# Optimization experiments

Hardware: AMD Instinct MI355X
Metric: run time of the kernel (lower is better)

Reference implementation:

```python
import jax, jax.numpy as jnp
import numpy as np

HEADS = 4
DIM_HEAD = 32


def setup_inputs() -> dict:
    key = jax.random.key(0)
    k1, k2, k3, k4 = jax.random.split(key, 4)
    dim = 128
    hidden = HEADS * DIM_HEAD  # 128
    x = jax.random.normal(k1, (32, dim, 64, 64), dtype=jnp.float32)
    w_qkv = jax.random.normal(k2, (3 * hidden, dim), dtype=jnp.float32) * (1.0 / np.sqrt(dim))
    w_out = jax.random.normal(k3, (dim, hidden), dtype=jnp.float32) * (1.0 / np.sqrt(hidden))
    b_out = jax.random.normal(k4, (dim,), dtype=jnp.float32) * 0.01
    return {"x": x, "w_qkv": w_qkv, "w_out": w_out, "b_out": b_out}


def reference(x, w_qkv, w_out, b_out):
    b, c, h, w = x.shape
    n = h * w
    # 1x1 conv (no bias) == channel matmul
    qkv = jnp.einsum('oc,bchw->bohw', w_qkv, x)  # [b, 3*heads*dh, h, w]
    qkv = qkv.reshape(b, 3, HEADS, DIM_HEAD, n)
    q, k, v = qkv[:, 0], qkv[:, 1], qkv[:, 2]  # each [b, heads, dh, n]
    k = jax.nn.softmax(k, axis=-1)  # softmax over spatial positions
    context = jnp.einsum('bhdn,bhen->bhde', k, v)  # [b, heads, dh, dh]
    out = jnp.einsum('bhde,bhdn->bhen', context, q)  # [b, heads, dh, n]
    out = out.reshape(b, HEADS * DIM_HEAD, h, w)
    # 1x1 conv with bias
    return jnp.einsum('oc,bchw->bohw', w_out, out) + b_out[None, :, None, None]
```

## Files before the change

kernel.cpp:

```cpp
#include <hip/hip_runtime.h>
#include <hip/hip_bf16.h>
#include <math.h>

#define BATCH 32
#define CDIM  128
#define NTOT  4096
#define NCH   32
#define CHN   128
#define TN    64
#define NCH3  16

typedef __attribute__((ext_vector_type(4))) float f32x4;
typedef __attribute__((ext_vector_type(8))) short s16x8;

#define PC_OFF  0
#define PC_SIZE (BATCH * 4 * NCH * 32 * 32)
#define PS_OFF  (PC_OFF + PC_SIZE)
#define PS_SIZE (BATCH * 4 * NCH * 32)
#define MBF_OFF (PS_OFF + PS_SIZE)
#define MBF_SIZE (BATCH * CDIM * CDIM / 2)
#define CTX_OFF (MBF_OFF + MBF_SIZE)
#define CTX_SIZE (BATCH * 4 * 1024)
#define XBT_OFF (CTX_OFF + CTX_SIZE)
#define XBT_SIZE (BATCH * CDIM * NTOT / 2)
#define NEED_BYTES ((size_t)(XBT_OFF + XBT_SIZE) * 4)

static __device__ __forceinline__ unsigned short f2bf(float f) {
    return __builtin_bit_cast(unsigned short, __float2bfloat16(f));
}
static __device__ __forceinline__ unsigned int pack2(float a, float b) {
    return (unsigned int)f2bf(a) | ((unsigned int)f2bf(b) << 16);
}
static __device__ __forceinline__ s16x8 ld_frag_lds(const unsigned int* p, int d0) {
    int4 t;
    t.x = (int)p[d0]; t.y = (int)p[d0 + 1];
    t.z = (int)p[d0 + 2]; t.w = (int)p[d0 + 3];
    return __builtin_bit_cast(s16x8, t);
}

static __device__ __forceinline__ void stage_xT(const float* __restrict__ xc,
                                                unsigned int* __restrict__ xsd,
                                                int tid) {
    const int m  = tid & 15;
    const int cg = tid >> 4;
#pragma unroll
    for (int p = 0; p < 4; ++p) {
        const int c = 2 * cg + 32 * p;
        const f32x4 a0 = *reinterpret_cast<const f32x4*>(xc + (size_t)c * NTOT + 4 * m);
        const f32x4 a1 = *reinterpret_cast<const f32x4*>(xc + (size_t)(c + 1) * NTOT + 4 * m);
#pragma unroll
        for (int jj = 0; jj < 4; ++jj)
            xsd[(4 * m + jj) * 65 + (c >> 1)] = pack2(a0[jj], a1[jj]);
    }
}

template <bool XBT>
__global__ __launch_bounds__(256, 2)
void k1_ctx(const float* __restrict__ x, const float* __restrict__ wqkv,
            float* __restrict__ ws) {
    __shared__ __attribute__((aligned(16))) unsigned short xsT[64 * 130];
    __shared__ __attribute__((aligned(16))) unsigned short ekv[8][32][72];

    const int j = blockIdx.x, b = blockIdx.y;
    const int tid = threadIdx.x;
    const int l = tid & 63;
    const int w = tid >> 6;
    const int m = l & 15, hq = l >> 4;

    s16x8 afr[4][4];
#pragma unroll
    for (int tm = 0; tm < 4; ++tm)
#pragma unroll
        for (int kt = 0; kt < 4; ++kt) {
            const float* wr = wqkv +
                (size_t)(CDIM + 64 * w + 16 * tm + m) * CDIM + 32 * kt + 8 * hq;
            const f32x4 u0 = *reinterpret_cast<const f32x4*>(wr);
            const f32x4 u1 = *reinterpret_cast<const f32x4*>(wr + 4);
            int4 t4;
            t4.x = (int)pack2(u0[0], u0[1]); t4.y = (int)pack2(u0[2], u0[3]);
            t4.z = (int)pack2(u1[0], u1[1]); t4.w = (int)pack2(u1[2], u1[3]);
            afr[tm][kt] = __builtin_bit_cast(s16x8, t4);
        }

    f32x4 cacc[2][2] = {};
    float sacc[4][4] = {};
    const float* xc = x + (size_t)b * CDIM * NTOT + j * CHN;
    unsigned int* xsd = (unsigned int*)xsT;

    for (int it = 0; it < CHN / TN; ++it) {
        stage_xT(xc + it * TN, xsd, tid);
        __syncthreads();

        f32x4 acc[4][4] = {};
#pragma unroll
        for (int kt = 0; kt < 4; ++kt) {
#pragma unroll
            for (int tn = 0; tn < 4; ++tn) {
                const s16x8 bfr = ld_frag_lds(xsd, (16 * tn + m) * 65 + 16 * kt + 4 * hq);
#pragma unroll
                for (int tm = 0; tm < 4; ++tm)
                    acc[tm][tn] = __builtin_amdgcn_mfma_f32_16x16x32_bf16(
                        afr[tm][kt], bfr, acc[tm][tn], 0, 0, 0);
            }
        }

        if constexpr (XBT) {
            unsigned int* tb = (unsigned int*)(ws + XBT_OFF) +
                               ((size_t)b * 64 + j * 2 + it) * 4096;
            const int n = tid >> 2, qt = tid & 3;
#pragma unroll
            for (int p = 0; p < 4; ++p) {
                const int cdl = 16 * p + 4 * qt;
                const int src = n * 65 + (cdl ^ ((n & 7) << 2));
                uint4 v;
                v.x = xsd[src]; v.y = xsd[src + 1];
                v.z = xsd[src + 2]; v.w = xsd[src + 3];
                *reinterpret_cast<uint4*>(tb + (size_t)n * 64 + cdl) = v;
            }
        }

        if (w < 2) {
#pragma unroll
            for (int tm = 0; tm < 4; ++tm)
#pragma unroll
                for (int tn = 0; tn < 4; ++tn)
#pragma unroll
                    for (int r = 0; r < 4; ++r) {
                        const int dg = 64 * w + 16 * tm + 4 * hq + r;
                        const float e = __expf(acc[tm][tn][r]);
                        sacc[tm][r] += e;
                        ekv[dg >> 5][dg & 31][16 * tn + m] = f2bf(e);
                    }
        } else {
#pragma unroll
            for (int tm = 0; tm < 4; ++tm)
#pragma unroll
                for (int tn = 0; tn < 4; ++tn)
#pragma unroll
                    for (int r = 0; r < 4; ++r) {
                        const int eg = 64 * (w - 2) + 16 * tm + 4 * hq + r;
                        ekv[4 + (eg >> 5)][eg & 31][16 * tn + m] = f2bf(acc[tm][tn][r]);
                    }
        }
        __syncthreads();

#pragma unroll
        for (int kt = 0; kt < 2; ++kt) {
            s16x8 va[2], eb[2];
#pragma unroll
            for (int t = 0; t < 2; ++t) {
                va[t] = *reinterpret_cast<const s16x8*>(
                    &ekv[4 + w][16 * t + m][32 * kt + 8 * hq]);
                eb[t] = *reinterpret_cast<const s16x8*>(
                    &ekv[w][16 * t + m][32 * kt + 8 * hq]);
            }
#pragma unroll
            for (int tm = 0; tm < 2; ++tm)
#pragma unroll
                for (int tn = 0; tn < 2; ++tn)
                    cacc[tm][tn] = __builtin_amdgcn_mfma_f32_16x16x32_bf16(
                        va[tm], eb[tn], cacc[tm][tn], 0, 0, 0);
        }
        __syncthreads();
    }

    float* pc = ws + PC_OFF + (size_t)((b * 4 + w) * NCH + j) * 1024;
#pragma unroll
    for (int tm = 0; tm < 2; ++tm)
#pragma unroll
        for (int tn = 0; tn < 2; ++tn)
#pragma unroll
            for (int r = 0; r < 4; ++r)
                pc[(16 * tm + 4 * hq + r) * 32 + 16 * tn + m] = cacc[tm][tn][r];

    if (w < 2) {
#pragma unroll
        for (int tm = 0; tm < 4; ++tm)
#pragma unroll
            for (int r = 0; r < 4; ++r) {
                float s = sacc[tm][r];
                s += __shfl_xor(s, 1);
                s += __shfl_xor(s, 2);
                s += __shfl_xor(s, 4);
                s += __shfl_xor(s, 8);
                if (m == 0) {
                    const int dg = 64 * w + 16 * tm + 4 * hq + r;
                    ws[PS_OFF + (size_t)((b * 4 + (dg >> 5)) * NCH + j) * 32 + (dg & 31)] = s;
                }
            }
    }
}

__global__ __launch_bounds__(256)
void k2a_ctx(float* __restrict__ ws) {
    const int bh = blockIdx.x;
    const int tid = threadIdx.x;
    __shared__ float stotS[32];
    if (tid < 32) {
        float s = 0.f;
#pragma unroll 8
        for (int jj = 0; jj < NCH; ++jj)
            s += ws[PS_OFF + (size_t)(bh * NCH + jj) * 32 + tid];
        stotS[tid] = s;
    }
    __syncthreads();
#pragma unroll
    for (int k = 0; k < 4; ++k) {
        const int idx = tid + 256 * k;
        float c = 0.f;
#pragma unroll 8
        for (int jj = 0; jj < NCH; ++jj)
            c += ws[PC_OFF + (size_t)(bh * NCH + jj) * 1024 + idx];
        ws[CTX_OFF + (size_t)bh * 1024 + idx] = c / stotS[idx & 31];
    }
}

__global__ __launch_bounds__(256)
void k2b_buildM(const float* __restrict__ wqkv, const float* __restrict__ wout,
                float* __restrict__ ws) {
    const int oq = blockIdx.x;
    const int b  = blockIdx.y;
    const int tid = threadIdx.x;

    __shared__ __attribute__((aligned(16))) float smA[8704];
    __shared__ float G[32][133];
    float* ctxs  = smA;
    float* wouts = smA + 4224;
    unsigned int* wqs = (unsigned int*)smA;

#pragma unroll
    for (int k = 0; k < 16; ++k) {
        const int fid = tid + 256 * k;
        const int h = fid >> 10, rem = fid & 1023;
        const int e = rem >> 5, d = rem & 31;
        ctxs[(h * 32 + d) * 33 + e] = ws[CTX_OFF + (size_t)b * 4096 + fid];
    }
#pragma unroll
    for (int k = 0; k < 16; ++k) {
        const int fid = tid + 256 * k;
        const int o = fid >> 7, c = fid & 127;
        wouts[o * 133 + c] = wout[(size_t)(oq * 32 + o) * CDIM + c];
    }
    __syncthreads();

    {
        const int o2 = tid & 31;
        const int g8 = tid >> 5;
#pragma unroll
        for (int i = 0; i < 16; ++i) {
            const int hd = g8 * 16 + i;
            const int h = hd >> 5;
            float acc = 0.f;
#pragma unroll
            for (int e = 0; e < 32; ++e)
                acc = fmaf(wouts[o2 * 133 + h * 32 + e], ctxs[hd * 33 + e], acc);
            G[o2][hd] = acc;
        }
    }
    __syncthreads();

    {
#pragma unroll
        for (int k = 0; k < 32; ++k) {
            const int fid = tid + 256 * k;
            const int hd = fid >> 6, cd = fid & 63;
            const float2 wv =
                *reinterpret_cast<const float2*>(wqkv + (size_t)hd * CDIM + 2 * cd);
            wqs[hd * 68 + cd] = pack2(wv.x, wv.y);
        }
    }
    __syncthreads();

    {
        const int o3 = tid >> 3;
        const int c0 = tid & 7;
        float Macc[16];
#pragma unroll
        for (int i = 0; i < 16; ++i) Macc[i] = 0.f;
        for (int hd = 0; hd < 128; ++hd) {
            const float gv = G[o3][hd];
            const uint4 w0 = *reinterpret_cast<const uint4*>(&wqs[hd * 68 + c0 * 8]);
            const uint4 w1 = *reinterpret_cast<const uint4*>(&wqs[hd * 68 + c0 * 8 + 4]);
            const unsigned int dw[8] = {w0.x, w0.y, w0.z, w0.w, w1.x, w1.y, w1.z, w1.w};
#pragma unroll
            for (int q = 0; q < 8; ++q) {
                const float lo = __builtin_bit_cast(float, dw[q] << 16);
                const float hi = __builtin_bit_cast(float, dw[q] & 0xffff0000u);
                Macc[2 * q]     = fmaf(gv, lo, Macc[2 * q]);
                Macc[2 * q + 1] = fmaf(gv, hi, Macc[2 * q + 1]);
            }
        }
        unsigned int* mpd = (unsigned int*)((unsigned short*)(ws + MBF_OFF) +
                                            (size_t)b * CDIM * CDIM) +
                            (oq * 32 + o3) * 64 + c0 * 8;
        uint4 s0, s1;
        s0.x = pack2(Macc[0], Macc[1]);   s0.y = pack2(Macc[2], Macc[3]);
        s0.z = pack2(Macc[4], Macc[5]);   s0.w = pack2(Macc[6], Macc[7]);
        s1.x = pack2(Macc[8], Macc[9]);   s1.y = pack2(Macc[10], Macc[11]);
        s1.z = pack2(Macc[12], Macc[13]); s1.w = pack2(Macc[14], Macc[15]);
        *reinterpret_cast<uint4*>(mpd) = s0;
        *reinterpret_cast<uint4*>(mpd + 4) = s1;
    }
}

template <bool XBT>
__global__ __launch_bounds__(256)
void k3_final(const float* __restrict__ x, const float* __restrict__ bout,
              const float* __restrict__ ws, float* __restrict__ out) {
    __shared__ __attribute__((aligned(16))) unsigned int xsd[4160];

    const int j = blockIdx.x, b = blockIdx.y;
    const int tid = threadIdx.x, l = tid & 63, w = tid >> 6;
    const int m = l & 15, hq = l >> 4;

    const unsigned short* mbf =
        (const unsigned short*)(ws + MBF_OFF) + (size_t)b * CDIM * CDIM;
    s16x8 afr[2][4];
#pragma unroll
    for (int tm = 0; tm < 2; ++tm)
#pragma unroll
        for (int kt = 0; kt < 4; ++kt)
            afr[tm][kt] = *reinterpret_cast<const s16x8*>(
                mbf + (size_t)(32 * w + 16 * tm + m) * CDIM + 32 * kt + 8 * hq);
    float bias[2][4];
#pragma unroll
    for (int tm = 0; tm < 2; ++tm)
#pragma unroll
        for (int r = 0; r < 4; ++r)
            bias[tm][r] = bout[32 * w + 16 * tm + 4 * hq + r];

    const float* xc = x + (size_t)b * CDIM * NTOT + j * 256;
    float* oc = out + (size_t)b * CDIM * NTOT + j * 256;
    const unsigned int* tb = (const unsigned int*)(ws + XBT_OFF) +
                             ((size_t)b * 64 + j * 4) * 4096;

    for (int it = 0; it < 4; ++it) {
        if constexpr (XBT) {
            const unsigned int* src = tb + it * 4096;
#pragma unroll
            for (int rep = 0; rep < 4; ++rep) {
                const int dw = rep * 1024 + tid * 4;
                *reinterpret_cast<uint4*>(&xsd[dw]) =
                    *reinterpret_cast<const uint4*>(src + dw);
            }
        } else {
            stage_xT(xc + it * TN, xsd, tid);
        }
        __syncthreads();

        f32x4 acc[2][4] = {};
#pragma unroll
        for (int kt = 0; kt < 4; ++kt) {
#pragma unroll
            for (int tn = 0; tn < 4; ++tn) {
                const int nl = 16 * tn + m;
                s16x8 bfr;
                if constexpr (XBT) {
                    const int idx = nl * 64 + ((16 * kt + 4 * hq) ^ ((nl & 7) << 2));
                    bfr = __builtin_bit_cast(
                        s16x8, *reinterpret_cast<const int4*>(&xsd[idx]));
                } else {
                    bfr = ld_frag_lds(xsd, nl * 65 + 16 * kt + 4 * hq);
                }
#pragma unroll
                for (int tm = 0; tm < 2; ++tm)
                    acc[tm][tn] = __builtin_amdgcn_mfma_f32_16x16x32_bf16(
                        afr[tm][kt], bfr, acc[tm][tn], 0, 0, 0);
            }
        }
#pragma unroll
        for (int tm = 0; tm < 2; ++tm)
#pragma unroll
            for (int tn = 0; tn < 4; ++tn)
#pragma unroll
                for (int r = 0; r < 4; ++r)
                    oc[(size_t)(32 * w + 16 * tm + 4 * hq + r) * NTOT +
                       it * TN + 16 * tn + m] = acc[tm][tn][r] + bias[tm][r];
        __syncthreads();
    }
}

extern "C" void kernel_launch(void* const* d_in, const int* in_sizes, int n_in,
                              void* d_out, int out_size, void* d_ws, size_t ws_size,
                              hipStream_t stream) {
    const float* x    = (const float*)d_in[0];
    const float* wqkv = (const float*)d_in[1];
    const float* wout = (const float*)d_in[2];
    const float* bout = (const float*)d_in[3];
    float* out = (float*)d_out;
    float* ws  = (float*)d_ws;

    const bool xbt = ws_size >= NEED_BYTES;

    if (xbt)
        k1_ctx<true><<<dim3(NCH, BATCH), 256, 0, stream>>>(x, wqkv, ws);
    else
        k1_ctx<false><<<dim3(NCH, BATCH), 256, 0, stream>>>(x, wqkv, ws);

    k2a_ctx<<<BATCH * 4, 256, 0, stream>>>(ws);
    k2b_buildM<<<dim3(4, BATCH), 256, 0, stream>>>(wqkv, wout, ws);

    if (xbt)
        k3_final<true><<<dim3(NCH3, BATCH), 256, 0, stream>>>(x, bout, ws, out);
    else
        k3_final<false><<<dim3(NCH3, BATCH), 256, 0, stream>>>(x, bout, ws, out);
}
```

Measured before the change: 87.93 us.

## Use 512-thread blocks with larger spatial chunks in context kernel

The context kernel now launches 512 threads per block (8 waves) over 256-wide spatial chunks, halving the grid. Each wave computes half as many QKV rows, so per-thread register use for fragments and accumulators drops. The context MFMA reduction is split across two waves per head, each doing one k-slice, which doubles the partial-context buffers that the reduction kernel has to sum. The aim is higher occupancy and cheaper per-block weight loading, at the cost of more partial-sum traffic.

After: 85.78 us. 1.03x faster.

```diff
diff --git a/kernel.cpp b/kernel.cpp
--- a/kernel.cpp
+++ b/kernel.cpp
@@ -5,8 +5,9 @@
 #define BATCH 32
 #define CDIM  128
 #define NTOT  4096
-#define NCH   32
-#define CHN   128
+#define NCH   16
+#define NCH2  (NCH * 2)
+#define CHN   256
 #define TN    64
 #define NCH3  16
 
@@ -14,7 +15,7 @@
 typedef __attribute__((ext_vector_type(8))) short s16x8;
 
 #define PC_OFF  0
-#define PC_SIZE (BATCH * 4 * NCH * 32 * 32)
+#define PC_SIZE (BATCH * 4 * NCH2 * 32 * 32)
 #define PS_OFF  (PC_OFF + PC_SIZE)
 #define PS_SIZE (BATCH * 4 * NCH * 32)
 #define MBF_OFF (PS_OFF + PS_SIZE)
@@ -55,7 +56,7 @@
 }
 
 template <bool XBT>
-__global__ __launch_bounds__(256, 2)
+__global__ __launch_bounds__(512)
 void k1_ctx(const float* __restrict__ x, const float* __restrict__ wqkv,
             float* __restrict__ ws) {
     __shared__ __attribute__((aligned(16))) unsigned short xsT[64 * 130];
@@ -66,14 +67,15 @@
     const int l = tid & 63;
     const int w = tid >> 6;
     const int m = l & 15, hq = l >> 4;
-
-    s16x8 afr[4][4];
-#pragma unroll
-    for (int tm = 0; tm < 4; ++tm)
+    const int m16 = tid & 15, cg = tid >> 4;
+
+    s16x8 afr[2][4];
+#pragma unroll
+    for (int tm = 0; tm < 2; ++tm)
 #pragma unroll
         for (int kt = 0; kt < 4; ++kt) {
             const float* wr = wqkv +
-                (size_t)(CDIM + 64 * w + 16 * tm + m) * CDIM + 32 * kt + 8 * hq;
+                (size_t)(CDIM + 32 * w + 16 * tm + m) * CDIM + 32 * kt + 8 * hq;
             const f32x4 u0 = *reinterpret_cast<const f32x4*>(wr);
             const f32x4 u1 = *reinterpret_cast<const f32x4*>(wr + 4);
             int4 t4;
@@ -83,22 +85,34 @@
         }
 
     f32x4 cacc[2][2] = {};
-    float sacc[4][4] = {};
+    float sacc[2][4] = {};
+    const int h  = w >> 1;
+    const int ks = w & 1;
     const float* xc = x + (size_t)b * CDIM * NTOT + j * CHN;
     unsigned int* xsd = (unsigned int*)xsT;
 
     for (int it = 0; it < CHN / TN; ++it) {
-        stage_xT(xc + it * TN, xsd, tid);
+#pragma unroll
+        for (int p = 0; p < 2; ++p) {
+            const int c = 2 * cg + 64 * p;
+            const f32x4 a0 = *reinterpret_cast<const f32x4*>(
+                xc + (size_t)(it * TN) + (size_t)c * NTOT + 4 * m16);
+            const f32x4 a1 = *reinterpret_cast<const f32x4*>(
+                xc + (size_t)(it * TN) + (size_t)(c + 1) * NTOT + 4 * m16);
+#pragma unroll
+            for (int jj = 0; jj < 4; ++jj)
+                xsd[(4 * m16 + jj) * 65 + (c >> 1)] = pack2(a0[jj], a1[jj]);
+        }
         __syncthreads();
 
-        f32x4 acc[4][4] = {};
+        f32x4 acc[2][4] = {};
 #pragma unroll
         for (int kt = 0; kt < 4; ++kt) {
 #pragma unroll
             for (int tn = 0; tn < 4; ++tn) {
                 const s16x8 bfr = ld_frag_lds(xsd, (16 * tn + m) * 65 + 16 * kt + 4 * hq);
 #pragma unroll
-                for (int tm = 0; tm < 4; ++tm)
+                for (int tm = 0; tm < 2; ++tm)
                     acc[tm][tn] = __builtin_amdgcn_mfma_f32_16x16x32_bf16(
                         afr[tm][kt], bfr, acc[tm][tn], 0, 0, 0);
             }
@@ -106,11 +120,11 @@
 
         if constexpr (XBT) {
             unsigned int* tb = (unsigned int*)(ws + XBT_OFF) +
-                               ((size_t)b * 64 + j * 2 + it) * 4096;
-            const int n = tid >> 2, qt = tid & 3;
-#pragma unroll
-            for (int p = 0; p < 4; ++p) {
-                const int cdl = 16 * p + 4 * qt;
+                               ((size_t)b * 64 + j * 4 + it) * 4096;
+            const int n = tid >> 3, qt = tid & 7;
+#pragma unroll
+            for (int p = 0; p < 2; ++p) {
+                const int cdl = 32 * p + 4 * qt;
                 const int src = n * 65 + (cdl ^ ((n & 7) << 2));
                 uint4 v;
                 v.x = xsd[src]; v.y = xsd[src + 1];
@@ -119,40 +133,39 @@
             }
         }
 
-        if (w < 2) {
-#pragma unroll
-            for (int tm = 0; tm < 4; ++tm)
+        if (w < 4) {
+#pragma unroll
+            for (int tm = 0; tm < 2; ++tm)
 #pragma unroll
                 for (int tn = 0; tn < 4; ++tn)
 #pragma unroll
                     for (int r = 0; r < 4; ++r) {
-                        const int dg = 64 * w + 16 * tm + 4 * hq + r;
+                        const int dg = 32 * w + 16 * tm + 4 * hq + r;
                         const float e = __expf(acc[tm][tn][r]);
                         sacc[tm][r] += e;
                         ekv[dg >> 5][dg & 31][16 * tn + m] = f2bf(e);
                     }
         } else {
 #pragma unroll
-            for (int tm = 0; tm < 4; ++tm)
+            for (int tm = 0; tm < 2; ++tm)
 #pragma unroll
                 for (int tn = 0; tn < 4; ++tn)
 #pragma unroll
                     for (int r = 0; r < 4; ++r) {
-                        const int eg = 64 * (w - 2) + 16 * tm + 4 * hq + r;
+                        const int eg = 32 * (w - 4) + 16 * tm + 4 * hq + r;
                         ekv[4 + (eg >> 5)][eg & 31][16 * tn + m] = f2bf(acc[tm][tn][r]);
                     }
         }
         __syncthreads();
 
-#pragma unroll
-        for (int kt = 0; kt < 2; ++kt) {
+        {
             s16x8 va[2], eb[2];
 #pragma unroll
             for (int t = 0; t < 2; ++t) {
                 va[t] = *reinterpret_cast<const s16x8*>(
-                    &ekv[4 + w][16 * t + m][32 * kt + 8 * hq]);
+                    &ekv[4 + h][16 * t + m][32 * ks + 8 * hq]);
                 eb[t] = *reinterpret_cast<const s16x8*>(
-                    &ekv[w][16 * t + m][32 * kt + 8 * hq]);
+                    &ekv[h][16 * t + m][32 * ks + 8 * hq]);
             }
 #pragma unroll
             for (int tm = 0; tm < 2; ++tm)
@@ -164,7 +177,7 @@
         __syncthreads();
     }
 
-    float* pc = ws + PC_OFF + (size_t)((b * 4 + w) * NCH + j) * 1024;
+    float* pc = ws + PC_OFF + (size_t)((b * 4 + h) * NCH2 + (j * 2 + ks)) * 1024;
 #pragma unroll
     for (int tm = 0; tm < 2; ++tm)
 #pragma unroll
@@ -173,9 +186,9 @@
             for (int r = 0; r < 4; ++r)
                 pc[(16 * tm + 4 * hq + r) * 32 + 16 * tn + m] = cacc[tm][tn][r];
 
-    if (w < 2) {
-#pragma unroll
-        for (int tm = 0; tm < 4; ++tm)
+    if (w < 4) {
+#pragma unroll
+        for (int tm = 0; tm < 2; ++tm)
 #pragma unroll
             for (int r = 0; r < 4; ++r) {
                 float s = sacc[tm][r];
@@ -184,7 +197,7 @@
                 s += __shfl_xor(s, 4);
                 s += __shfl_xor(s, 8);
                 if (m == 0) {
-                    const int dg = 64 * w + 16 * tm + 4 * hq + r;
+                    const int dg = 32 * w + 16 * tm + 4 * hq + r;
                     ws[PS_OFF + (size_t)((b * 4 + (dg >> 5)) * NCH + j) * 32 + (dg & 31)] = s;
                 }
             }
@@ -209,8 +222,8 @@
         const int idx = tid + 256 * k;
         float c = 0.f;
 #pragma unroll 8
-        for (int jj = 0; jj < NCH; ++jj)
-            c += ws[PC_OFF + (size_t)(bh * NCH + jj) * 1024 + idx];
+        for (int jj = 0; jj < NCH2; ++jj)
+            c += ws[PC_OFF + (size_t)(bh * NCH2 + jj) * 1024 + idx];
         ws[CTX_OFF + (size_t)bh * 1024 + idx] = c / stotS[idx & 31];
     }
 }
@@ -393,9 +406,9 @@
     const bool xbt = ws_size >= NEED_BYTES;
 
     if (xbt)
-        k1_ctx<true><<<dim3(NCH, BATCH), 256, 0, stream>>>(x, wqkv, ws);
+        k1_ctx<true><<<dim3(NCH, BATCH), 512, 0, stream>>>(x, wqkv, ws);
     else
-        k1_ctx<false><<<dim3(NCH, BATCH), 256, 0, stream>>>(x, wqkv, ws);
+        k1_ctx<false><<<dim3(NCH, BATCH), 512, 0, stream>>>(x, wqkv, ws);
 
     k2a_ctx<<<BATCH * 4, 256, 0, stream>>>(ws);
     k2b_buildM<<<dim3(4, BATCH), 256, 0, stream>>>(wqkv, wout, ws);
```
